# Kernel optimization log

Hardware: AMD Instinct MI355X
Metric: run time of the kernel (lower is better)

## Reference

```python
import jax, jax.numpy as jnp
import numpy as np

H = 512      # hidden_size (hardcoded in prior split)
L = 3        # num_layers
NH = 8       # num_heads
B = 16384    # batch
LN_EPS = 1e-5


def layer_norm(x, g, b):
    m = x.mean(-1, keepdims=True)
    v = ((x - m) ** 2).mean(-1, keepdims=True)
    return (x - m) / jnp.sqrt(v + LN_EPS) * g + b


def cross_gen(src, tgt, ipw, ipb, qkv_w, qkv_b, ao_w, ao_b,
              ln1g, ln1b, ln2g, ln2b, f1w, f1b, f2w, f2b, opw, opb, rw):
    """CrossModalGenerator.forward(src, tgt) for the whole batch (seq_len == 1)."""
    bsz = src.shape[0]
    dh = H // NH
    x = src @ ipw.T + ipb  # input_proj
    for l in range(L):
        wq, wk, wv = jnp.split(qkv_w[l], 3, axis=0)
        bq, bk, bv = jnp.split(qkv_b[l], 3)
        q = (x @ wq.T + bq).reshape(bsz, NH, dh)
        k = (tgt @ wk.T + bk).reshape(bsz, NH, dh)
        v = (tgt @ wv.T + bv).reshape(bsz, NH, dh)
        # single key/value token -> softmax over 1 element == 1 (kept for faithful grads)
        scores = (q * k).sum(-1, keepdims=True) / jnp.sqrt(jnp.float32(dh))  # [B,NH,1]
        w = jax.nn.softmax(scores, axis=-1)
        attn = (w * v).reshape(bsz, H)
        attn = attn @ ao_w[l].T + ao_b[l]  # MHA out_proj
        x = layer_norm(x + attn, ln1g[l], ln1b[l])
        h = jax.nn.gelu(x @ f1w[l].T + f1b[l], approximate=False)
        h = h @ f2w[l].T + f2b[l]
        x = layer_norm(x + h, ln2g[l], ln2b[l])
    gen = x @ opw.T + opb  # output_proj
    return rw * tgt + (1.0 - rw) * gen


def setup_inputs() -> dict:
    key = jax.random.key(0)
    ks = iter(jax.random.split(key, 40))
    nk = lambda: next(ks)
    s = jnp.float32(0.02)  # weight scale for numerical sanity
    f32 = jnp.float32
    return {
        "image_features": jax.random.normal(nk(), (B, H), f32),
        "text_features": jax.random.normal(nk(), (B, H), f32),
        "g_ipw": jax.random.normal(nk(), (2, H, H), f32) * s,
        "g_ipb": jnp.zeros((2, H), f32),
        "g_qkv_w": jax.random.normal(nk(), (2, L, 3 * H, H), f32) * s,
        "g_qkv_b": jnp.zeros((2, L, 3 * H), f32),
        "g_ao_w": jax.random.normal(nk(), (2, L, H, H), f32) * s,
        "g_ao_b": jnp.zeros((2, L, H), f32),
        "g_ln1g": jnp.ones((2, L, H), f32),
        "g_ln1b": jnp.zeros((2, L, H), f32),
        "g_ln2g": jnp.ones((2, L, H), f32),
        "g_ln2b": jnp.zeros((2, L, H), f32),
        "g_f1w": jax.random.normal(nk(), (2, L, 4 * H, H), f32) * s,
        "g_f1b": jnp.zeros((2, L, 4 * H), f32),
        "g_f2w": jax.random.normal(nk(), (2, L, H, 4 * H), f32) * s,
        "g_f2b": jnp.zeros((2, L, H), f32),
        "g_opw": jax.random.normal(nk(), (2, H, H), f32) * s,
        "g_opb": jnp.zeros((2, H), f32),
        "g_rw": jnp.full((2,), 0.5, f32),  # residual_weight per generator
        "prior_w1": jax.random.normal(nk(), (2 * H, H), f32) * s,
        "prior_b1": jnp.zeros((2 * H,), f32),
        "prior_w2": jax.random.normal(nk(), (2 * H, 2 * H), f32) * s,
        "prior_b2": jnp.zeros((2 * H,), f32),
        "prior_emb": jax.random.normal(nk(), (1, H), f32),
        "missing_type": jax.random.randint(nk(), (B,), 0, 4, jnp.int32),
    }


def reference(image_features, text_features, g_ipw, g_ipb, g_qkv_w, g_qkv_b,
              g_ao_w, g_ao_b, g_ln1g, g_ln1b, g_ln2g, g_ln2b, g_f1w, g_f1b,
              g_f2w, g_f2b, g_opw, g_opb, g_rw, prior_w1, prior_b1, prior_w2,
              prior_b2, prior_emb, missing_type):
    def gen(i, src, tgt):
        return cross_gen(src, tgt, g_ipw[i], g_ipb[i], g_qkv_w[i], g_qkv_b[i],
                         g_ao_w[i], g_ao_b[i], g_ln1g[i], g_ln1b[i],
                         g_ln2g[i], g_ln2b[i], g_f1w[i], g_f1b[i],
                         g_f2w[i], g_f2b[i], g_opw[i], g_opb[i], g_rw[i])

    # MoE-style dense dispatch: run both generators on the full batch, select by type.
    gen_text = gen(0, image_features, text_features)  # img_to_text, missing_type==1
    gen_img = gen(1, text_features, image_features)   # text_to_img, missing_type==2

    prior = jax.nn.gelu(prior_emb @ prior_w1.T + prior_b1, approximate=False)
    prior = prior @ prior_w2.T + prior_b2  # [1, 2H]
    p_img, p_text = prior[:, :H], prior[:, H:]

    mt = missing_type[:, None]
    enhanced_img = jnp.where(mt == 2, gen_img, image_features)
    enhanced_img = jnp.where(mt == 3, p_img, enhanced_img)
    enhanced_text = jnp.where(mt == 1, gen_text, text_features)
    enhanced_text = jnp.where(mt == 3, p_text, enhanced_text)
    return enhanced_img, enhanced_text
```

## Files before the change

### kernel.cpp

```cpp
#include <hip/hip_runtime.h>
#include <hip/hip_bf16.h>
#include <math.h>

#define BDIM 16384
#define HDIM 512

typedef __bf16 bf16;
typedef float f32x4 __attribute__((ext_vector_type(4)));
typedef __bf16 bf16x8 __attribute__((ext_vector_type(8)));
typedef __bf16 bf16x4 __attribute__((ext_vector_type(4)));

#define WAITV(N) asm volatile("s_waitcnt vmcnt(" #N ")" ::: "memory")


__device__ __forceinline__ void gload16(const bf16* g, bf16* l) {
  __builtin_amdgcn_global_load_lds((const __attribute__((address_space(1))) void*)g,
                                   (__attribute__((address_space(3))) void*)l, 16, 0, 0);
}

__device__ __forceinline__ float gelu_exact(float x) {
  return 0.5f * x * (1.0f + erff(x * 0.70710678118654752f));
}
__device__ __forceinline__ float gelu_fast2(float x) {
  float x3 = x * x * x;
  float e = exp2f(fmaf(-0.1029432f, x3, -2.3022082f * x));
  return x * __builtin_amdgcn_rcpf(1.f + e);
}


__global__ void cvt_f32_bf16(const float* __restrict__ src, bf16* __restrict__ dst, int n4) {
  int i = blockIdx.x * blockDim.x + threadIdx.x;
  if (i >= n4) return;
  f32x4 v = *(const f32x4*)(src + (size_t)i * 4);
  bf16x4 o;
  o[0] = (bf16)v[0]; o[1] = (bf16)v[1]; o[2] = (bf16)v[2]; o[3] = (bf16)v[3];
  *(bf16x4*)(dst + (size_t)i * 4) = o;
}

__global__ void cvt_cat(const float* __restrict__ img, const float* __restrict__ txt,
                        bf16* __restrict__ cat) {
  int i = blockIdx.x * 256 + threadIdx.x;
  int r = i >> 7;
  int c = (i & 127) << 3;
  const float* s = (c < 512) ? (img + (size_t)r * 512 + c)
                             : (txt + (size_t)r * 512 + (c - 512));
  f32x4 v0 = *(const f32x4*)s;
  f32x4 v1 = *(const f32x4*)(s + 4);
  bf16x8 o;
#pragma unroll
  for (int j = 0; j < 4; ++j) { o[j] = (bf16)v0[j]; o[4 + j] = (bf16)v1[j]; }
  *(bf16x8*)(cat + (size_t)r * 1024 + c) = o;
}

__global__ void cat_w(const bf16* __restrict__ ipw_bf, const bf16* __restrict__ Wc_bf,
                      bf16* __restrict__ Wcat) {
  int i = blockIdx.x * 256 + threadIdx.x;
  int g = i >> 16;
  int rem = i & 65535;
  int n = rem >> 7;
  int c = (rem & 127) << 3;
  const bf16* s;
  if (g == 0) s = (c < 512) ? (ipw_bf + (size_t)n * 512 + c)
                            : (Wc_bf + (size_t)n * 512 + (c - 512));
  else        s = (c < 512) ? (Wc_bf + (size_t)3 * 262144 + (size_t)n * 512 + c)
                            : (ipw_bf + 262144 + (size_t)n * 512 + (c - 512));
  *(bf16x8*)(Wcat + (size_t)g * 524288 + (size_t)n * 1024 + c) = *(const bf16x8*)s;
}

__global__ void bcat_k(const float* __restrict__ ipb, const float* __restrict__ bc,
                       float* __restrict__ bcat) {
  int i = blockIdx.x * 256 + threadIdx.x;
  int g = i >> 9, n = i & 511;
  bcat[i] = ipb[g * 512 + n] + bc[g * 1536 + n];
}

__global__ void cvt_wvT(const float* __restrict__ qkv, bf16* __restrict__ dst) {
  __shared__ float t[32][33];
  int il = blockIdx.z;
  int bm = blockIdx.x * 32;
  int bk = blockIdx.y * 32;
  const float* s = qkv + (size_t)il * 786432 + 524288;
  int tx = threadIdx.x & 31, ty = threadIdx.x >> 5;
#pragma unroll
  for (int j = 0; j < 4; ++j)
    t[ty * 4 + j][tx] = s[(size_t)(bm + ty * 4 + j) * 512 + bk + tx];
  __syncthreads();
  bf16* d = dst + (size_t)il * 262144;
#pragma unroll
  for (int j = 0; j < 4; ++j)
    d[(size_t)(bk + ty * 4 + j) * 512 + bm + tx] = (bf16)t[tx][ty * 4 + j];
}

__global__ void zfill(float* __restrict__ p, int n) {
  int i = blockIdx.x * 256 + threadIdx.x;
  if (i < n) p[i] = 0.f;
}

__global__ void bias_combine(const float* __restrict__ aow, const float* __restrict__ qkvb,
                             const float* __restrict__ aob, float* __restrict__ bc) {
  int gid = blockIdx.x * 4 + (threadIdx.x >> 6);
  int il = gid >> 9;
  int lane = threadIdx.x & 63;
  const float* ar = aow + (size_t)gid * 512 + lane * 8;
  const float* bv = qkvb + il * 1536 + 1024 + lane * 8;
  float s = 0.f;
#pragma unroll
  for (int i = 0; i < 8; ++i) s += ar[i] * bv[i];
#pragma unroll
  for (int off = 32; off > 0; off >>= 1) s += __shfl_xor(s, off);
  if (lane == 0) bc[gid] = s + aob[gid];
}


template<int ACT, bool RES, int K, int FIN>
__launch_bounds__(512, 1)
__global__ void gemm_8p(const bf16* __restrict__ A, long long Az, int lda,
                        const bf16* __restrict__ W, long long Wz,
                        const float* __restrict__ bias, long long bz,
                        const bf16* X, long long Xz,
                        bf16* C, long long Cz, int ldc,
                        const float* imgF, const float* txtF,
                        const float* prior, const int* mt,
                        const float* rwp, float* outF) {
  __shared__ bf16 lds[65536];
  const long long z = blockIdx.z;
  A += z * Az; W += z * Wz; bias += z * bz; C += z * Cz;
  if (RES) X += z * Xz;
  const int tid = threadIdx.x, lane = tid & 63, wid = tid >> 6;
  const int brow = blockIdx.x * 256, bcol = blockIdx.y * 256;
  const int wm = (wid >> 2) * 128;
  const int wn = (wid & 3) * 64;
  const int lr = lane & 15, kg = lane >> 4;
  const int ko = (kg ^ ((lr >> 1) & 3)) << 3;

  f32x4 acc[8][4] = {};

  const int sco = (((tid & 3) ^ ((tid >> 3) & 3)) << 3);
  const bf16* Ag = A + (size_t)(brow + (tid >> 2)) * lda + sco;
  const bf16* Wg = W + (size_t)(bcol + (tid >> 2)) * K + sco;
  const int nt = K / 64;

  auto STG = [&](const bf16* gbase, int kt, int kh, int dstE, int rstride) {
    int ck = kt < nt ? kt : nt - 1;
    const bf16* s = gbase + (size_t)ck * 64 + (size_t)kh * 32;
    gload16(s, lds + dstE + wid * 512);
    gload16(s + (size_t)128 * rstride, lds + dstE + 4096 + wid * 512);
  };

  STG(Ag, 0, 0, 0, lda);         STG(Wg, 0, 0, 16384, K);
  STG(Ag, 0, 1, 8192, lda);      STG(Wg, 0, 1, 24576, K);
  STG(Ag, 1, 0, 32768, lda);     STG(Wg, 1, 0, 49152, K);

  bf16x8 a[8], b01[2], b23[2];

#define RD_A(BASE)                                                             \
  { _Pragma("unroll") for (int m = 0; m < 8; ++m)                              \
      a[m] = *(const bf16x8*)(lds + (BASE) + ((wm + m * 16 + lr) << 5) + ko); }
#define RD_B01(BASE)                                                           \
  { b01[0] = *(const bf16x8*)(lds + (BASE) + ((wn + lr) << 5) + ko);           \
    b01[1] = *(const bf16x8*)(lds + (BASE) + ((wn + 16 + lr) << 5) + ko); }
#define RD_B23(BASE)                                                           \
  { b23[0] = *(const bf16x8*)(lds + (BASE) + ((wn + 32 + lr) << 5) + ko);      \
    b23[1] = *(const bf16x8*)(lds + (BASE) + ((wn + 48 + lr) << 5) + ko); }
#define MM(N0, BB)                                                             \
  { __builtin_amdgcn_s_setprio(1);                                             \
    _Pragma("unroll") for (int m = 0; m < 8; ++m) {                            \
      acc[m][N0]     = __builtin_amdgcn_mfma_f32_16x16x32_bf16(BB[0], a[m], acc[m][N0], 0, 0, 0);     \
      acc[m][N0 + 1] = __builtin_amdgcn_mfma_f32_16x16x32_bf16(BB[1], a[m], acc[m][N0 + 1], 0, 0, 0); } \
    __builtin_amdgcn_s_setprio(0); }
#define BARW                                                                   \
  WAITV(6); __builtin_amdgcn_s_barrier(); asm volatile("" ::: "memory");
#define ENDP                                                                   \
  asm volatile("" ::: "memory"); __builtin_amdgcn_s_barrier();

  BARW
  RD_A(0) RD_B01(16384)

  const int niter = nt / 2;
  for (int i = 0; i < niter; ++i) {
    const int t = 2 * i;
    STG(Ag, t + 1, 1, 40960, lda);
    BARW  MM(0, b01)  RD_B23(16384)                      ENDP
    STG(Wg, t + 1, 1, 57344, K);
    BARW  MM(2, b23)  RD_A(8192) RD_B01(24576)           ENDP
    STG(Ag, t + 2, 0, 0, lda);
    BARW  MM(0, b01)  RD_B23(24576)                      ENDP
    STG(Wg, t + 2, 0, 16384, K);
    BARW  MM(2, b23)  RD_A(32768) RD_B01(49152)          ENDP
    STG(Ag, t + 2, 1, 8192, lda);
    BARW  MM(0, b01)  RD_B23(49152)                      ENDP
    STG(Wg, t + 2, 1, 24576, K);
    BARW  MM(2, b23)  RD_A(40960) RD_B01(57344)          ENDP
    STG(Ag, t + 3, 0, 32768, lda);
    BARW  MM(0, b01)  RD_B23(57344)                      ENDP
    STG(Wg, t + 3, 0, 49152, K);
    BARW  MM(2, b23)  RD_A(0) RD_B01(16384)              ENDP
  }
#undef RD_A
#undef RD_B01
#undef RD_B23
#undef MM
#undef BARW
#undef ENDP

  f32x4 bv4[4];
#pragma unroll
  for (int n = 0; n < 4; ++n)
    bv4[n] = *(const f32x4*)(bias + bcol + wn + n * 16 + kg * 4);

  if constexpr (FIN == 1) {
    float r = rwp[z];
    const float* basep = z ? imgF : txtF;
    const float* pr = prior + (z ? 0 : 512);
    float* op2 = outF + (z ? (size_t)0 : (size_t)BDIM * HDIM);
    const int want = z ? 2 : 1;
#pragma unroll
    for (int m = 0; m < 8; ++m) {
      int row = brow + wm + m * 16 + lr;
      int msel = mt[row];
#pragma unroll
      for (int n = 0; n < 4; ++n) {
        int col = bcol + wn + n * 16 + kg * 4;
        f32x4 base4 = *(const f32x4*)(basep + (size_t)row * 512 + col);
        f32x4 o;
#pragma unroll
        for (int j = 0; j < 4; ++j) {
          float g = acc[m][n][j] + bv4[n][j];
          float ov = base4[j];
          if (msel == want) ov = r * base4[j] + (1.f - r) * g;
          else if (msel == 3) ov = pr[col + j];
          o[j] = ov;
        }
        *(f32x4*)(op2 + (size_t)row * 512 + col) = o;
      }
    }
    return;
  }

#pragma unroll
  for (int m = 0; m < 8; ++m) {
    int row = brow + wm + m * 16 + lr;
#pragma unroll
    for (int n = 0; n < 4; ++n) {
      int col = bcol + wn + n * 16 + kg * 4;
      f32x4 v;
#pragma unroll
      for (int j = 0; j < 4; ++j) {
        float t2 = acc[m][n][j] + bv4[n][j];
        if (ACT == 1) t2 = gelu_fast2(t2);
        v[j] = t2;
      }
      if (RES) {
        bf16x4 xv = *(const bf16x4*)(X + (size_t)row * 512 + col);
#pragma unroll
        for (int j = 0; j < 4; ++j) v[j] += (float)xv[j];
      }
      bf16x4 o;
#pragma unroll
      for (int j = 0; j < 4; ++j) o[j] = (bf16)v[j];
      *(bf16x4*)(C + (size_t)row * ldc + col) = o;
    }
  }
}


template<int MODE>
__global__ void ln_chain(const bf16* __restrict__ Y, const bf16* __restrict__ R,
                         const float* __restrict__ gA, const float* __restrict__ bA,
                         const float* __restrict__ gB, const float* __restrict__ bB,
                         bf16* __restrict__ O) {
  int lane = threadIdx.x & 63;
  int row = blockIdx.x * 4 + (threadIdx.x >> 6);
  int gen = row >> 14;
  size_t base = (size_t)row * HDIM + lane * 8;
  bf16x8 yv = *(const bf16x8*)(Y + base);
  float v[8], s = 0.f, q = 0.f;
#pragma unroll
  for (int i = 0; i < 8; ++i) { v[i] = (float)yv[i]; s += v[i]; q += v[i] * v[i]; }
#pragma unroll
  for (int off = 32; off > 0; off >>= 1) { s += __shfl_xor(s, off); q += __shfl_xor(q, off); }
  float mean = s * (1.f / HDIM);
  float rstd = rsqrtf(q * (1.f / HDIM) - mean * mean + 1e-5f);
  const float* gAp = gA + gen * 1536 + lane * 8;
  const float* bAp = bA + gen * 1536 + lane * 8;
  if (MODE == 0) {
    bf16x8 o;
#pragma unroll
    for (int i = 0; i < 8; ++i) o[i] = (bf16)((v[i] - mean) * rstd * gAp[i] + bAp[i]);
    *(bf16x8*)(O + base) = o;
    return;
  }
  bf16x8 rv = *(const bf16x8*)(R + base);
  float u[8]; s = 0.f; q = 0.f;
#pragma unroll
  for (int i = 0; i < 8; ++i) {
    u[i] = (v[i] - mean) * rstd * gAp[i] + bAp[i] + (float)rv[i];
    s += u[i]; q += u[i] * u[i];
  }
#pragma unroll
  for (int off = 32; off > 0; off >>= 1) { s += __shfl_xor(s, off); q += __shfl_xor(q, off); }
  float m2 = s * (1.f / HDIM);
  float r2 = rsqrtf(q * (1.f / HDIM) - m2 * m2 + 1e-5f);
  const float* gBp = gB + gen * 1536 + lane * 8;
  const float* bBp = bB + gen * 1536 + lane * 8;
  bf16x8 o;
#pragma unroll
  for (int i = 0; i < 8; ++i) o[i] = (bf16)((u[i] - m2) * r2 * gBp[i] + bBp[i]);
  *(bf16x8*)(O + base) = o;
}


__launch_bounds__(256)
__global__ void gemm128(const bf16* __restrict__ A, long long Az, int lda,
                        const bf16* __restrict__ W, long long Wz,
                        const float* __restrict__ bias, long long bz,
                        bf16* __restrict__ C, long long Cz, int ldc, int K) {
  __shared__ bf16 As[128 * 64];
  __shared__ bf16 Bs[128 * 64];
  const long long z = blockIdx.z;
  A += z * Az; W += z * Wz; bias += z * bz; C += z * Cz;
  const int tid = threadIdx.x;
  const int lane = tid & 63;
  const int wid = tid >> 6;
  const int brow = blockIdx.x * 128;
  const int bcol = blockIdx.y * 128;
  const int wr = (wid >> 1) * 64;
  const int wc = (wid & 1) * 64;
  const int lr = lane & 15;
  const int kg = lane >> 4;
  f32x4 acc[4][4] = {};
  const bf16* Abase = A + (size_t)(brow + (tid >> 3)) * lda + ((tid & 7) << 3);
  const bf16* Wbase = W + (size_t)(bcol + (tid >> 3)) * K + ((tid & 7) << 3);
  bf16* AsDst = As + wid * 512;
  bf16* BsDst = Bs + wid * 512;
  for (int k0 = 0; k0 < K; k0 += 64) {
#pragma unroll
    for (int j = 0; j < 4; ++j) {
      gload16(Abase + (size_t)j * 32 * lda + k0, AsDst + j * 2048);
      gload16(Wbase + (size_t)j * 32 * K + k0, BsDst + j * 2048);
    }
    __syncthreads();
#pragma unroll
    for (int kk = 0; kk < 64; kk += 32) {
      bf16x8 a[4], bq[4];
#pragma unroll
      for (int m = 0; m < 4; ++m)
        a[m] = *(const bf16x8*)(As + (wr + m * 16 + lr) * 64 + kk + kg * 8);
#pragma unroll
      for (int n = 0; n < 4; ++n)
        bq[n] = *(const bf16x8*)(Bs + (wc + n * 16 + lr) * 64 + kk + kg * 8);
#pragma unroll
      for (int m = 0; m < 4; ++m)
#pragma unroll
        for (int n = 0; n < 4; ++n)
          acc[m][n] = __builtin_amdgcn_mfma_f32_16x16x32_bf16(a[m], bq[n], acc[m][n], 0, 0, 0);
    }
    __syncthreads();
  }
  float bv[4];
#pragma unroll
  for (int n = 0; n < 4; ++n) bv[n] = bias[bcol + wc + n * 16 + lr];
#pragma unroll
  for (int m = 0; m < 4; ++m) {
    int row = brow + wr + m * 16 + kg * 4;
#pragma unroll
    for (int n = 0; n < 4; ++n) {
      int col = bcol + wc + n * 16 + lr;
#pragma unroll
      for (int j = 0; j < 4; ++j)
        C[(size_t)(row + j) * ldc + col] = (bf16)(acc[m][n][j] + bv[n]);
    }
  }
}


__global__ void prior_fc1(const float* __restrict__ emb, const float* __restrict__ w1,
                          const float* __restrict__ b1, float* __restrict__ h) {
  int j = blockIdx.x * 4 + (threadIdx.x >> 6);
  int lane = threadIdx.x & 63;
  const float* wr = w1 + (size_t)j * 512 + lane * 8;
  const float* e = emb + lane * 8;
  float s = 0.f;
#pragma unroll
  for (int i = 0; i < 8; ++i) s += e[i] * wr[i];
#pragma unroll
  for (int off = 32; off > 0; off >>= 1) s += __shfl_xor(s, off);
  if (lane == 0) h[j] = gelu_exact(s + b1[j]);
}

__global__ void prior_fc2(const float* __restrict__ h, const float* __restrict__ w2,
                          const float* __restrict__ b2, float* __restrict__ p) {
  int j = blockIdx.x * 4 + (threadIdx.x >> 6);
  int lane = threadIdx.x & 63;
  const float* wr = w2 + (size_t)j * 1024 + lane * 16;
  const float* e = h + lane * 16;
  float s = 0.f;
#pragma unroll
  for (int i = 0; i < 16; ++i) s += e[i] * wr[i];
#pragma unroll
  for (int off = 32; off > 0; off >>= 1) s += __shfl_xor(s, off);
  if (lane == 0) p[j] = s + b2[j];
}


extern "C" void kernel_launch(void* const* d_in, const int* in_sizes, int n_in,
                              void* d_out, int out_size, void* d_ws, size_t ws_size,
                              hipStream_t stream) {
  const float* img  = (const float*)d_in[0];
  const float* txt  = (const float*)d_in[1];
  const float* ipw  = (const float*)d_in[2];
  const float* ipb  = (const float*)d_in[3];
  const float* qkvw = (const float*)d_in[4];
  const float* qkvb = (const float*)d_in[5];
  const float* aow  = (const float*)d_in[6];
  const float* aob  = (const float*)d_in[7];
  const float* ln1g = (const float*)d_in[8];
  const float* ln1b = (const float*)d_in[9];
  const float* ln2g = (const float*)d_in[10];
  const float* ln2b = (const float*)d_in[11];
  const float* f1w  = (const float*)d_in[12];
  const float* f1b  = (const float*)d_in[13];
  const float* f2w  = (const float*)d_in[14];
  const float* f2b  = (const float*)d_in[15];
  const float* opw  = (const float*)d_in[16];
  const float* opb  = (const float*)d_in[17];
  const float* rw   = (const float*)d_in[18];
  const float* pw1  = (const float*)d_in[19];
  const float* pb1  = (const float*)d_in[20];
  const float* pw2  = (const float*)d_in[21];
  const float* pb2  = (const float*)d_in[22];
  const float* pemb = (const float*)d_in[23];
  const int*   mt   = (const int*)d_in[24];
  float* out = (float*)d_out;

  const size_t B = BDIM;
  char* ws = (char*)d_ws;
  size_t off = 0;
  auto alloc = [&](size_t bytes) -> char* {
    char* p = ws + off;
    off += (bytes + 255) & ~(size_t)255;
    return p;
  };
  bf16* cat    = (bf16*)alloc((size_t)B * 1024 * 2);
  bf16* ipw_bf = (bf16*)alloc((size_t)2 * 262144 * 2);
  bf16* wvT_bf = (bf16*)alloc((size_t)6 * 262144 * 2);
  bf16* ao_bf  = (bf16*)alloc((size_t)6 * 262144 * 2);
  bf16* f1_bf  = (bf16*)alloc((size_t)6 * 1048576 * 2);
  bf16* f2_bf  = (bf16*)alloc((size_t)6 * 1048576 * 2);
  bf16* op_bf  = (bf16*)alloc((size_t)2 * 262144 * 2);
  bf16* Wc_bf  = (bf16*)alloc((size_t)6 * 262144 * 2);
  bf16* Wcat   = (bf16*)alloc((size_t)2 * 524288 * 2);
  float* bc    = (float*)alloc(6 * 512 * 4);
  float* bcat  = (float*)alloc(1024 * 4);
  float* zeros = (float*)alloc(512 * 4);
  float* ph    = (float*)alloc(1024 * 4);
  float* pout  = (float*)alloc(1024 * 4);
  bf16* xn     = (bf16*)alloc(2 * B * 512 * 2);
  bf16* hreg   = (bf16*)alloc((size_t)B * 2048 * 2);
  bf16* h0     = (bf16*)d_out;
  const long long HZ = (long long)(hreg - h0);

  auto cvt = [&](const float* s, bf16* d, size_t n) {
    int n4 = (int)(n / 4);
    cvt_f32_bf16<<<(n4 + 255) / 256, 256, 0, stream>>>(s, d, n4);
  };
  cvt_cat<<<8192, 256, 0, stream>>>(img, txt, cat);
  cvt(ipw, ipw_bf, 2 * 262144);
  cvt(aow, ao_bf, 6 * 262144);
  cvt(f1w, f1_bf, 6 * 1048576);
  cvt(f2w, f2_bf, 6 * 1048576);
  cvt(opw, op_bf, 2 * 262144);
  cvt_wvT<<<dim3(16, 16, 6), 256, 0, stream>>>(qkvw, wvT_bf);
  zfill<<<2, 256, 0, stream>>>(zeros, 512);
  bias_combine<<<768, 256, 0, stream>>>(aow, qkvb, aob, bc);
  gemm128<<<dim3(4, 4, 6), 256, 0, stream>>>(ao_bf, 262144, 512, wvT_bf, 262144,
                                             zeros, 0, Wc_bf, 262144, 512, 512);
  cat_w<<<512, 256, 0, stream>>>(ipw_bf, Wc_bf, Wcat);
  bcat_k<<<4, 256, 0, stream>>>(ipb, bc, bcat);
  prior_fc1<<<256, 256, 0, stream>>>(pemb, pw1, pb1, ph);
  prior_fc2<<<256, 256, 0, stream>>>(ph, pw2, pb2, pout);

  const long long BS = (long long)B * 512;

  auto attn = [&](int l) {
    gemm_8p<0, false, 512, 0><<<dim3(64, 2, 2), 512, 0, stream>>>(
        cat + 512, -512, 1024, Wc_bf + (size_t)l * 262144, 786432,
        bc + l * 512, 1536, nullptr, 0, hreg, BS, 512,
        nullptr, nullptr, nullptr, nullptr, nullptr, nullptr);
  };

  gemm_8p<0, false, 1024, 0><<<dim3(64, 2, 2), 512, 0, stream>>>(
      cat, 0, 1024, Wcat, 524288, bcat, 512, nullptr, 0, xn, BS, 512,
      nullptr, nullptr, nullptr, nullptr, nullptr, nullptr);
  ln_chain<0><<<2 * BDIM / 4, 256, 0, stream>>>(xn, nullptr, ln1g, ln1b,
                                                nullptr, nullptr, xn);

  for (int l = 0; l < 3; ++l) {
    gemm_8p<1, false, 512, 0><<<dim3(64, 8, 2), 512, 0, stream>>>(
        xn, BS, 512, f1_bf + (size_t)l * 1048576, 3145728,
        f1b + l * 2048, 6144, nullptr, 0, h0, HZ, 2048,
        nullptr, nullptr, nullptr, nullptr, nullptr, nullptr);
    gemm_8p<0, true, 2048, 0><<<dim3(64, 2, 2), 512, 0, stream>>>(
        h0, HZ, 2048, f2_bf + (size_t)l * 1048576, 3145728,
        f2b + l * 512, 1536, xn, BS, xn, BS, 512,
        nullptr, nullptr, nullptr, nullptr, nullptr, nullptr);
    if (l < 2) {
      attn(l + 1);
      ln_chain<1><<<2 * BDIM / 4, 256, 0, stream>>>(
          xn, hreg, ln2g + l * 512, ln2b + l * 512,
          ln1g + (l + 1) * 512, ln1b + (l + 1) * 512, xn);
    } else {
      ln_chain<0><<<2 * BDIM / 4, 256, 0, stream>>>(
          xn, nullptr, ln2g + l * 512, ln2b + l * 512, nullptr, nullptr, xn);
    }
  }

  gemm_8p<0, false, 512, 1><<<dim3(64, 2, 2), 512, 0, stream>>>(
      xn, BS, 512, op_bf, 262144, opb, 512, nullptr, 0, hreg, BS, 512,
      img, txt, pout, mt, rw, out);
}
```

Baseline: 819.1 us.

## Use 4-wave 256-thread GEMM blocks with 128x128 per-wave tiles

The main bf16 GEMM kernel now runs with 256 threads (4 waves) per block instead of 512 (8 waves). Each wave computes a 128x128 output tile with an 8x8 grid of MFMA accumulators, and each thread issues four global-to-LDS loads per stage instead of two. The wait count is raised to match. This doubles per-wave operand reuse and halves LDS B-reads per MFMA, but it doubles accumulator registers per wave and halves the number of waves available to hide latency.

```diff
diff --git a/kernel.cpp b/kernel.cpp
--- a/kernel.cpp
+++ b/kernel.cpp
@@ -113,27 +113,27 @@
 
 
 template<int ACT, bool RES, int K, int FIN>
-__launch_bounds__(512, 1)
-__global__ void gemm_8p(const bf16* __restrict__ A, long long Az, int lda,
-                        const bf16* __restrict__ W, long long Wz,
-                        const float* __restrict__ bias, long long bz,
-                        const bf16* X, long long Xz,
-                        bf16* C, long long Cz, int ldc,
-                        const float* imgF, const float* txtF,
-                        const float* prior, const int* mt,
-                        const float* rwp, float* outF) {
+__launch_bounds__(256, 1)
+__global__ void gemm_w(const bf16* __restrict__ A, long long Az, int lda,
+                       const bf16* __restrict__ W, long long Wz,
+                       const float* __restrict__ bias, long long bz,
+                       const bf16* X, long long Xz,
+                       bf16* C, long long Cz, int ldc,
+                       const float* imgF, const float* txtF,
+                       const float* prior, const int* mt,
+                       const float* rwp, float* outF) {
   __shared__ bf16 lds[65536];
   const long long z = blockIdx.z;
   A += z * Az; W += z * Wz; bias += z * bz; C += z * Cz;
   if (RES) X += z * Xz;
   const int tid = threadIdx.x, lane = tid & 63, wid = tid >> 6;
   const int brow = blockIdx.x * 256, bcol = blockIdx.y * 256;
-  const int wm = (wid >> 2) * 128;
-  const int wn = (wid & 3) * 64;
+  const int wm = (wid >> 1) * 128;
+  const int wn = (wid & 1) * 128;
   const int lr = lane & 15, kg = lane >> 4;
   const int ko = (kg ^ ((lr >> 1) & 3)) << 3;
 
-  f32x4 acc[8][4] = {};
+  f32x4 acc[8][8] = {};
 
   const int sco = (((tid & 3) ^ ((tid >> 3) & 3)) << 3);
   const bf16* Ag = A + (size_t)(brow + (tid >> 2)) * lda + sco;
@@ -143,69 +143,66 @@
   auto STG = [&](const bf16* gbase, int kt, int kh, int dstE, int rstride) {
     int ck = kt < nt ? kt : nt - 1;
     const bf16* s = gbase + (size_t)ck * 64 + (size_t)kh * 32;
-    gload16(s, lds + dstE + wid * 512);
-    gload16(s + (size_t)128 * rstride, lds + dstE + 4096 + wid * 512);
+#pragma unroll
+    for (int j = 0; j < 4; ++j)
+      gload16(s + (size_t)j * 64 * rstride, lds + dstE + j * 2048 + wid * 512);
   };
 
   STG(Ag, 0, 0, 0, lda);         STG(Wg, 0, 0, 16384, K);
   STG(Ag, 0, 1, 8192, lda);      STG(Wg, 0, 1, 24576, K);
   STG(Ag, 1, 0, 32768, lda);     STG(Wg, 1, 0, 49152, K);
 
-  bf16x8 a[8], b01[2], b23[2];
+  bf16x8 a[8], b[4];
 
 #define RD_A(BASE)                                                             \
   { _Pragma("unroll") for (int m = 0; m < 8; ++m)                              \
       a[m] = *(const bf16x8*)(lds + (BASE) + ((wm + m * 16 + lr) << 5) + ko); }
-#define RD_B01(BASE)                                                           \
-  { b01[0] = *(const bf16x8*)(lds + (BASE) + ((wn + lr) << 5) + ko);           \
-    b01[1] = *(const bf16x8*)(lds + (BASE) + ((wn + 16 + lr) << 5) + ko); }
-#define RD_B23(BASE)                                                           \
-  { b23[0] = *(const bf16x8*)(lds + (BASE) + ((wn + 32 + lr) << 5) + ko);      \
-    b23[1] = *(const bf16x8*)(lds + (BASE) + ((wn + 48 + lr) << 5) + ko); }
-#define MM(N0, BB)                                                             \
+#define RD_B(BASE, NG)                                                         \
+  { _Pragma("unroll") for (int n = 0; n < 4; ++n)                              \
+      b[n] = *(const bf16x8*)(lds + (BASE) + ((wn + (NG * 4 + n) * 16 + lr) << 5) + ko); }
+#define MM(NG)                                                                 \
   { __builtin_amdgcn_s_setprio(1);                                             \
-    _Pragma("unroll") for (int m = 0; m < 8; ++m) {                            \
-      acc[m][N0]     = __builtin_amdgcn_mfma_f32_16x16x32_bf16(BB[0], a[m], acc[m][N0], 0, 0, 0);     \
-      acc[m][N0 + 1] = __builtin_amdgcn_mfma_f32_16x16x32_bf16(BB[1], a[m], acc[m][N0 + 1], 0, 0, 0); } \
+    _Pragma("unroll") for (int m = 0; m < 8; ++m)                              \
+      _Pragma("unroll") for (int n = 0; n < 4; ++n)                            \
+        acc[m][NG * 4 + n] = __builtin_amdgcn_mfma_f32_16x16x32_bf16(b[n], a[m], acc[m][NG * 4 + n], 0, 0, 0); \
     __builtin_amdgcn_s_setprio(0); }
 #define BARW                                                                   \
-  WAITV(6); __builtin_amdgcn_s_barrier(); asm volatile("" ::: "memory");
+  WAITV(12); __builtin_amdgcn_s_barrier(); asm volatile("" ::: "memory");
 #define ENDP                                                                   \
   asm volatile("" ::: "memory"); __builtin_amdgcn_s_barrier();
 
   BARW
-  RD_A(0) RD_B01(16384)
+  RD_A(0) RD_B(16384, 0)
 
   const int niter = nt / 2;
   for (int i = 0; i < niter; ++i) {
     const int t = 2 * i;
     STG(Ag, t + 1, 1, 40960, lda);
-    BARW  MM(0, b01)  RD_B23(16384)                      ENDP
+    BARW  MM(0)  RD_B(16384, 1)                ENDP
     STG(Wg, t + 1, 1, 57344, K);
-    BARW  MM(2, b23)  RD_A(8192) RD_B01(24576)           ENDP
+    BARW  MM(1)  RD_A(8192) RD_B(24576, 0)     ENDP
     STG(Ag, t + 2, 0, 0, lda);
-    BARW  MM(0, b01)  RD_B23(24576)                      ENDP
+    BARW  MM(0)  RD_B(24576, 1)                ENDP
     STG(Wg, t + 2, 0, 16384, K);
-    BARW  MM(2, b23)  RD_A(32768) RD_B01(49152)          ENDP
+    BARW  MM(1)  RD_A(32768) RD_B(49152, 0)    ENDP
     STG(Ag, t + 2, 1, 8192, lda);
-    BARW  MM(0, b01)  RD_B23(49152)                      ENDP
+    BARW  MM(0)  RD_B(49152, 1)                ENDP
     STG(Wg, t + 2, 1, 24576, K);
-    BARW  MM(2, b23)  RD_A(40960) RD_B01(57344)          ENDP
+    BARW  MM(1)  RD_A(40960) RD_B(57344, 0)    ENDP
     STG(Ag, t + 3, 0, 32768, lda);
-    BARW  MM(0, b01)  RD_B23(57344)                      ENDP
+    BARW  MM(0)  RD_B(57344, 1)                ENDP
     STG(Wg, t + 3, 0, 49152, K);
-    BARW  MM(2, b23)  RD_A(0) RD_B01(16384)              ENDP
+    BARW  MM(1)  RD_A(0) RD_B(16384, 0)        ENDP
   }
 #undef RD_A
-#undef RD_B01
-#undef RD_B23
+#undef RD_B
 #undef MM
 #undef BARW
 #undef ENDP
 
-  f32x4 bv4[4];
-#pragma unroll
-  for (int n = 0; n < 4; ++n)
+  f32x4 bv4[8];
+#pragma unroll
+  for (int n = 0; n < 8; ++n)
     bv4[n] = *(const f32x4*)(bias + bcol + wn + n * 16 + kg * 4);
 
   if constexpr (FIN == 1) {
@@ -219,7 +216,7 @@
       int row = brow + wm + m * 16 + lr;
       int msel = mt[row];
 #pragma unroll
-      for (int n = 0; n < 4; ++n) {
+      for (int n = 0; n < 8; ++n) {
         int col = bcol + wn + n * 16 + kg * 4;
         f32x4 base4 = *(const f32x4*)(basep + (size_t)row * 512 + col);
         f32x4 o;
@@ -241,7 +238,7 @@
   for (int m = 0; m < 8; ++m) {
     int row = brow + wm + m * 16 + lr;
 #pragma unroll
-    for (int n = 0; n < 4; ++n) {
+    for (int n = 0; n < 8; ++n) {
       int col = bcol + wn + n * 16 + kg * 4;
       f32x4 v;
 #pragma unroll
@@ -483,24 +480,24 @@
   const long long BS = (long long)B * 512;
 
   auto attn = [&](int l) {
-    gemm_8p<0, false, 512, 0><<<dim3(64, 2, 2), 512, 0, stream>>>(
+    gemm_w<0, false, 512, 0><<<dim3(64, 2, 2), 256, 0, stream>>>(
         cat + 512, -512, 1024, Wc_bf + (size_t)l * 262144, 786432,
         bc + l * 512, 1536, nullptr, 0, hreg, BS, 512,
         nullptr, nullptr, nullptr, nullptr, nullptr, nullptr);
   };
 
-  gemm_8p<0, false, 1024, 0><<<dim3(64, 2, 2), 512, 0, stream>>>(
+  gemm_w<0, false, 1024, 0><<<dim3(64, 2, 2), 256, 0, stream>>>(
       cat, 0, 1024, Wcat, 524288, bcat, 512, nullptr, 0, xn, BS, 512,
       nullptr, nullptr, nullptr, nullptr, nullptr, nullptr);
   ln_chain<0><<<2 * BDIM / 4, 256, 0, stream>>>(xn, nullptr, ln1g, ln1b,
                                                 nullptr, nullptr, xn);
 
   for (int l = 0; l < 3; ++l) {
-    gemm_8p<1, false, 512, 0><<<dim3(64, 8, 2), 512, 0, stream>>>(
+    gemm_w<1, false, 512, 0><<<dim3(64, 8, 2), 256, 0, stream>>>(
         xn, BS, 512, f1_bf + (size_t)l * 1048576, 3145728,
         f1b + l * 2048, 6144, nullptr, 0, h0, HZ, 2048,
         nullptr, nullptr, nullptr, nullptr, nullptr, nullptr);
-    gemm_8p<0, true, 2048, 0><<<dim3(64, 2, 2), 512, 0, stream>>>(
+    gemm_w<0, true, 2048, 0><<<dim3(64, 2, 2), 256, 0, stream>>>(
         h0, HZ, 2048, f2_bf + (size_t)l * 1048576, 3145728,
         f2b + l * 512, 1536, xn, BS, xn, BS, 512,
         nullptr, nullptr, nullptr, nullptr, nullptr, nullptr);
@@ -515,7 +512,7 @@
     }
   }
 
-  gemm_8p<0, false, 512, 1><<<dim3(64, 2, 2), 512, 0, stream>>>(
+  gemm_w<0, false, 512, 1><<<dim3(64, 2, 2), 256, 0, stream>>>(
       xn, BS, 512, op_bf, 262144, opb, 512, nullptr, 0, hreg, BS, 512,
       img, txt, pout, mt, rw, out);
 }
```

New measurement: 977.8 us. 19.4% more time.
